# Performance work log

Measured on AMD Instinct MI355X. Metric: run time of the kernel, lower is better.

The kernel has to match this reference:

```python
import jax, jax.numpy as jnp
import numpy as np

B, C, H = 16, 256, 128   # batch, channels (in==out, depthwise), spatial
K, S, P = 3, 2, 1        # kernel, stride, padding (the shape-consistent _Transition config)
LEAVES = 4               # levels=2 -> levels**2


def dwconv(x, w, b, stride, pad):
    # depthwise conv: w is [C,1,K,K] (torch OIHW with groups=C)
    out = jax.lax.conv_general_dilated(
        x, w, (stride, stride), [(pad, pad), (pad, pad)],
        dimension_numbers=('NCHW', 'OIHW', 'NCHW'),
        feature_group_count=x.shape[1])
    return out + b[None, :, None, None]


def maxpool(x, k, s, p):
    # matches nn.MaxPool2d (padding acts as -inf for max)
    return jax.lax.reduce_window(
        x, -jnp.inf, jax.lax.max,
        (1, 1, k, k), (1, 1, s, s),
        [(0, 0), (0, 0), (p, p), (p, p)])


def setup_inputs() -> dict:
    key = jax.random.key(0)
    k0, k1, k2, k3 = jax.random.split(key, 4)
    std = (2.0 / (K * K * C)) ** 0.5  # matches the module's normal_(0, sqrt(2/n)) init
    x = jax.random.normal(k0, (B, C, H, H), jnp.float32)
    maxgate = jax.random.normal(k1, (C, 1, K, K), jnp.float32) * std
    pconvs = jax.random.normal(k2, (C, 1, K, K, LEAVES), jnp.float32) * std  # dw=True
    pgates = jax.random.normal(k3, (C, 1, K, K, 3), jnp.float32) * std       # b=False: (leaves+levels)//2 = 3
    mb = jnp.zeros((C,), jnp.float32)
    pbs = jnp.zeros((C, LEAVES), jnp.float32)
    gbs = jnp.zeros((C, 3), jnp.float32)
    return dict(x=x, maxgate=maxgate, mb=mb, pconvs=pconvs, pbs=pbs,
                pgates=pgates, gbs=gbs)


def reference(x, maxgate, mb, pconvs, pbs, pgates, gbs):
    # max branch: maxpool * depthwise gate conv
    out = maxpool(x, K, S, P) * dwconv(x, maxgate, mb, S, P)

    # leaf stage: 2 sigmoid-gated pool pairs (b=False -> gate2 = 1 - gate1)
    # NOTE: code indexes pgates.select(4, c*2) with gbs.select(1, c)
    leaves = []
    for c in range(LEAVES // 2):
        g1 = jax.nn.sigmoid(dwconv(x, pgates[..., 2 * c], gbs[:, c], S, P))
        p1 = dwconv(x, pconvs[..., 2 * c], pbs[:, 2 * c], S, P)
        p2 = dwconv(x, pconvs[..., 2 * c + 1], pbs[:, 2 * c + 1], S, P)
        leaves.append(g1 * p1)
        leaves.append((1.0 - g1) * p2)

    n0 = leaves[0] + leaves[1]
    n1 = leaves[2] + leaves[3]

    # node stage (kernel_size==3 -> no F.pad); b=False reuses pgates[..., leaves//2 + n] = pgates[...,2]
    g = jax.nn.sigmoid(dwconv(n0, pgates[..., LEAVES // 2], gbs[:, 2], 1, P))
    out = out + n0 * g + n1 * (1.0 - g)
    return out
```

## Files before the change

kernel.cpp:

```cpp
#include <hip/hip_runtime.h>
#include <math.h>

#define TB   256
#define HH   128
#define OHW  64
#define TR   16
#define XR   37
#define N0C  68
#define NBLK (16 * 256 * 4)
#define CPX  (NBLK / 8)

typedef float f32x2 __attribute__((ext_vector_type(2)));

__device__ __forceinline__ float sigmoidf(float z) {
    return 1.0f / (1.0f + __expf(-z));
}

__device__ __forceinline__ void gl2lds16(const float* g, float* l) {
    __builtin_amdgcn_global_load_lds(
        (const __attribute__((address_space(1))) void*)g,
        (__attribute__((address_space(3))) void*)l, 16, 0, 0);
}
__device__ __forceinline__ void gl2lds4(const float* g, float* l) {
    __builtin_amdgcn_global_load_lds(
        (const __attribute__((address_space(1))) void*)g,
        (__attribute__((address_space(3))) void*)l, 4, 0, 0);
}

__global__ __launch_bounds__(TB, 6) void fused_densenet_kernel(
    const float* __restrict__ x,
    const float* __restrict__ maxgate,
    const float* __restrict__ mb,
    const float* __restrict__ pconvs,
    const float* __restrict__ pbs,
    const float* __restrict__ pgates,
    const float* __restrict__ gbs,
    float* __restrict__ out)
{
    __shared__ float xs[XR][HH];
    __shared__ float n0s[TR + 2][N0C];

    const int t     = threadIdx.x;
    const int lane  = t & 63;
    const int wv    = t >> 6;
    const int bid   = blockIdx.x;
    const int l     = (bid & 7) * CPX + (bid >> 3);
    const int tile  = l & 3;
    const int plane = l >> 2;
    const int c     = plane & 255;
    const int r0    = tile * TR;

    float ws[7][9];
#pragma unroll
    for (int i = 0; i < 9; ++i) {
        ws[0][i] = maxgate[c * 9  + i];
        ws[1][i] = pconvs [c * 36 + i * 4 + 0];
        ws[2][i] = pconvs [c * 36 + i * 4 + 1];
        ws[3][i] = pconvs [c * 36 + i * 4 + 2];
        ws[4][i] = pconvs [c * 36 + i * 4 + 3];
        ws[5][i] = pgates [c * 27 + i * 3 + 0];
        ws[6][i] = pgates [c * 27 + i * 3 + 2];
    }
    const float bmax = mb[c];
    const float bp0 = pbs[c * 4 + 0], bp1 = pbs[c * 4 + 1];
    const float bp2 = pbs[c * 4 + 2], bp3 = pbs[c * 4 + 3];
    const float bg0 = gbs[c * 3 + 0];
    const float bg1 = gbs[c * 3 + 1];
    const float bg2 = gbs[c * 3 + 2];

    const float* xplane = x + (size_t)plane * (HH * HH);

    {
        const int ir0  = 2 * r0 - 3;
        const int lo   = ir0 < 0 ? 0 : ir0;
        const int hie  = ir0 + XR - 1;
        const int hi   = hie > HH - 1 ? HH - 1 : hie;
        const int ztop = lo - ir0;
        const int zbot = hie - hi;
        for (int i = t; i < ztop * HH; i += TB) (&xs[0][0])[i] = 0.f;
        for (int i = t; i < zbot * HH; i += TB) (&xs[XR - zbot][0])[i] = 0.f;
        const int    nfl  = (hi - lo + 1) * HH;
        const float* gsrc = xplane + lo * HH;
        float*       ldst = &xs[ztop][0];
        const int nchunk = nfl >> 8;
        for (int k = wv; k < nchunk; k += TB / 64)
            gl2lds16(gsrc + (k << 8) + lane * 4, ldst + (k << 8));
        if ((nfl & 255) && wv == 0) {
            const int off = nchunk << 8;
            gl2lds4(gsrc + off + lane,      ldst + off);
            gl2lds4(gsrc + off + 64 + lane, ldst + off + 64);
        }
        if (t < 2 * (TR + 2)) n0s[t >> 1][(t & 1) ? 66 : 1] = 0.f;
    }
    __syncthreads();

    if (t < 132) {
        const int hb  = (t >= 66);
        const int cc2 = hb ? t - 66 : t;
        const int gc  = cc2 - 1;
        const int gr  = hb ? r0 + TR : r0 - 1;
        float n0v = 0.f;
        if ((unsigned)gr < (unsigned)OHW && (unsigned)gc < (unsigned)OHW) {
            const int sb = hb ? 2 * TR + 2 : 0;
            float ag = 0.f, a0 = 0.f, a1 = 0.f;
#pragma unroll
            for (int dr = 0; dr < 3; ++dr) {
                const float* row = &xs[sb + dr][0];
                const float w0 = (gc > 0) ? row[2 * gc - 1] : 0.f;
                const float w1 = row[2 * gc];
                const float w2 = row[2 * gc + 1];
                ag += w0 * ws[5][3*dr] + w1 * ws[5][3*dr+1] + w2 * ws[5][3*dr+2];
                a0 += w0 * ws[1][3*dr] + w1 * ws[1][3*dr+1] + w2 * ws[1][3*dr+2];
                a1 += w0 * ws[2][3*dr] + w1 * ws[2][3*dr+1] + w2 * ws[2][3*dr+2];
            }
            const float sg = sigmoidf(ag + bg0);
            n0v = sg * (a0 + bp0) + (1.f - sg) * (a1 + bp1);
        }
        n0s[hb ? TR + 1 : 0][cc2 + 1] = n0v;
    }

    const int p  = t & 31;
    const int g0 = t >> 5;
    float out1[2][2], n1v[2][2];

#pragma unroll
    for (int k = 0; k < 2; ++k) {
        const int lr = g0 + 8 * k;
        const int gr = r0 + lr;
        float a[7][2];
#pragma unroll
        for (int ci = 0; ci < 7; ++ci) { a[ci][0] = 0.f; a[ci][1] = 0.f; }
        float mp0 = -INFINITY, mp1 = -INFINITY;
#pragma unroll
        for (int dr = 0; dr < 3; ++dr) {
            const float* row = &xs[2 * lr + 2 + dr][0];
            const float  v0 = (p > 0) ? row[4 * p - 1] : 0.f;
            const float4 vv = *reinterpret_cast<const float4*>(&row[4 * p]);
            const bool rowok = (gr > 0) | (dr > 0);
            const float h0 = fmaxf(fmaxf((p > 0) ? v0 : -INFINITY, vv.x), vv.y);
            const float h1 = fmaxf(fmaxf(vv.y, vv.z), vv.w);
            mp0 = fmaxf(mp0, rowok ? h0 : -INFINITY);
            mp1 = fmaxf(mp1, rowok ? h1 : -INFINITY);
#pragma unroll
            for (int ci = 0; ci < 7; ++ci) {
                a[ci][0] += v0   * ws[ci][3*dr] + vv.x * ws[ci][3*dr+1] + vv.y * ws[ci][3*dr+2];
                a[ci][1] += vv.y * ws[ci][3*dr] + vv.z * ws[ci][3*dr+1] + vv.w * ws[ci][3*dr+2];
            }
        }
        const float sg0a = sigmoidf(a[5][0] + bg0);
        const float sg0b = sigmoidf(a[5][1] + bg0);
        const float n0a = sg0a * (a[1][0] + bp0) + (1.f - sg0a) * (a[2][0] + bp1);
        const float n0b = sg0b * (a[1][1] + bp0) + (1.f - sg0b) * (a[2][1] + bp1);
        *reinterpret_cast<f32x2*>(&n0s[lr + 1][2 * p + 2]) = (f32x2){ n0a, n0b };
        const float sg1a = sigmoidf(a[6][0] + bg1);
        const float sg1b = sigmoidf(a[6][1] + bg1);
        n1v[k][0] = sg1a * (a[3][0] + bp2) + (1.f - sg1a) * (a[4][0] + bp3);
        n1v[k][1] = sg1b * (a[3][1] + bp2) + (1.f - sg1b) * (a[4][1] + bp3);
        out1[k][0] = mp0 * (a[0][0] + bmax);
        out1[k][1] = mp1 * (a[0][1] + bmax);
    }
    __syncthreads();

    float* oplane = out + (size_t)plane * (OHW * OHW);
#pragma unroll
    for (int k = 0; k < 2; ++k) {
        const int lr = g0 + 8 * k;
        float ag0 = 0.f, ag1 = 0.f, n0c0 = 0.f, n0c1 = 0.f;
#pragma unroll
        for (int dr = 0; dr < 3; ++dr) {
            const float e0  = n0s[lr + dr][2 * p + 1];
            const f32x2 mid = *reinterpret_cast<const f32x2*>(&n0s[lr + dr][2 * p + 2]);
            const float e3  = n0s[lr + dr][2 * p + 4];
            ag0 += e0    * ws[6][3*dr] + mid.x * ws[6][3*dr+1] + mid.y * ws[6][3*dr+2];
            ag1 += mid.x * ws[6][3*dr] + mid.y * ws[6][3*dr+1] + e3    * ws[6][3*dr+2];
            if (dr == 1) { n0c0 = mid.x; n0c1 = mid.y; }
        }
        const float ga = sigmoidf(ag0 + bg2);
        const float gb = sigmoidf(ag1 + bg2);
        f32x2 rv;
        rv.x = out1[k][0] + n0c0 * ga + n1v[k][0] * (1.f - ga);
        rv.y = out1[k][1] + n0c1 * gb + n1v[k][1] * (1.f - gb);
        __builtin_nontemporal_store(rv,
            reinterpret_cast<f32x2*>(oplane + (r0 + lr) * OHW + 2 * p));
    }
}

extern "C" void kernel_launch(void* const* d_in, const int* in_sizes, int n_in,
                              void* d_out, int out_size, void* d_ws, size_t ws_size,
                              hipStream_t stream) {
    const float* x       = (const float*)d_in[0];
    const float* maxgate = (const float*)d_in[1];
    const float* mb      = (const float*)d_in[2];
    const float* pconvs  = (const float*)d_in[3];
    const float* pbs     = (const float*)d_in[4];
    const float* pgates  = (const float*)d_in[5];
    const float* gbs     = (const float*)d_in[6];
    float* out           = (float*)d_out;

    fused_densenet_kernel<<<NBLK, TB, 0, stream>>>(
        x, maxgate, mb, pconvs, pbs, pgates, gbs, out);
}
```

Before: 81.29 us.

## Give each wavefront its own private x row slab to drop the load barrier

Each wave now loads its own overlapping slice of input rows into LDS (40 rows instead of 37, with duplicated halo rows). It waits only on its own vmcnt, which removes the first __syncthreads. The thread mapping also changes from 2 output columns per thread over 2 strided rows to 1 column per thread over 4 consecutive rows. Halo n0 rows are computed by waves 0 and 3 instead of a separate thread subset. This trades extra LDS traffic and redundant row loads for less block-wide synchronization and better wave independence.

After: 86.54 us. 6.5% more time.

```diff
diff --git a/kernel.cpp b/kernel.cpp
--- a/kernel.cpp
+++ b/kernel.cpp
@@ -5,7 +5,6 @@
 #define HH   128
 #define OHW  64
 #define TR   16
-#define XR   37
 #define N0C  68
 #define NBLK (16 * 256 * 4)
 #define CPX  (NBLK / 8)
@@ -37,11 +36,11 @@
     const float* __restrict__ gbs,
     float* __restrict__ out)
 {
-    __shared__ float xs[XR][HH];
+    __shared__ float xs[40][HH];
     __shared__ float n0s[TR + 2][N0C];
 
     const int t     = threadIdx.x;
-    const int lane  = t & 63;
+    const int cc    = t & 63;
     const int wv    = t >> 6;
     const int bid   = blockIdx.x;
     const int l     = (bid & 7) * CPX + (bid >> 3);
@@ -70,118 +69,119 @@
 
     const float* xplane = x + (size_t)plane * (HH * HH);
 
+    const int  wbase = (wv == 0) ? 0 : (11 + 9 * (wv - 1));
+    const int  ib0   = 2 * r0 + 8 * wv - ((wv == 0) ? 3 : 1);
+    const int  nw    = (wv == 0 || wv == 3) ? 11 : 9;
+    float*     base  = &xs[wbase][0];
     {
-        const int ir0  = 2 * r0 - 3;
-        const int lo   = ir0 < 0 ? 0 : ir0;
-        const int hie  = ir0 + XR - 1;
+        const int lo   = ib0 < 0 ? 0 : ib0;
+        const int hie  = ib0 + nw - 1;
         const int hi   = hie > HH - 1 ? HH - 1 : hie;
-        const int ztop = lo - ir0;
+        const int ztop = lo - ib0;
         const int zbot = hie - hi;
-        for (int i = t; i < ztop * HH; i += TB) (&xs[0][0])[i] = 0.f;
-        for (int i = t; i < zbot * HH; i += TB) (&xs[XR - zbot][0])[i] = 0.f;
+        for (int r = 0; r < ztop; ++r)
+            *reinterpret_cast<f32x2*>(&base[r * HH + 2 * cc]) = (f32x2){0.f, 0.f};
+        for (int r = 0; r < zbot; ++r)
+            *reinterpret_cast<f32x2*>(&base[(nw - 1 - r) * HH + 2 * cc]) = (f32x2){0.f, 0.f};
         const int    nfl  = (hi - lo + 1) * HH;
         const float* gsrc = xplane + lo * HH;
-        float*       ldst = &xs[ztop][0];
+        float*       ldst = base + ztop * HH;
         const int nchunk = nfl >> 8;
-        for (int k = wv; k < nchunk; k += TB / 64)
-            gl2lds16(gsrc + (k << 8) + lane * 4, ldst + (k << 8));
-        if ((nfl & 255) && wv == 0) {
+        for (int k = 0; k < nchunk; ++k)
+            gl2lds16(gsrc + (k << 8) + cc * 4, ldst + (k << 8));
+        if (nfl & 255) {
             const int off = nchunk << 8;
-            gl2lds4(gsrc + off + lane,      ldst + off);
-            gl2lds4(gsrc + off + 64 + lane, ldst + off + 64);
-        }
-        if (t < 2 * (TR + 2)) n0s[t >> 1][(t & 1) ? 66 : 1] = 0.f;
-    }
-    __syncthreads();
-
-    if (t < 132) {
-        const int hb  = (t >= 66);
-        const int cc2 = hb ? t - 66 : t;
-        const int gc  = cc2 - 1;
-        const int gr  = hb ? r0 + TR : r0 - 1;
+            gl2lds4(gsrc + off + cc,      ldst + off);
+            gl2lds4(gsrc + off + 64 + cc, ldst + off + 64);
+        }
+    }
+    if (wv == 1 && cc < 2 * (TR + 2)) n0s[cc >> 1][(cc & 1) ? 66 : 1] = 0.f;
+
+    asm volatile("s_waitcnt vmcnt(0)" ::: "memory");
+
+    const int roff = (wv == 0) ? 2 : 0;
+
+    if (wv == 0) {
         float n0v = 0.f;
-        if ((unsigned)gr < (unsigned)OHW && (unsigned)gc < (unsigned)OHW) {
-            const int sb = hb ? 2 * TR + 2 : 0;
-            float ag = 0.f, a0 = 0.f, a1 = 0.f;
+        if (r0 > 0) {
+            float ag = 0.f, q0 = 0.f, q1 = 0.f;
 #pragma unroll
             for (int dr = 0; dr < 3; ++dr) {
-                const float* row = &xs[sb + dr][0];
-                const float w0 = (gc > 0) ? row[2 * gc - 1] : 0.f;
-                const float w1 = row[2 * gc];
-                const float w2 = row[2 * gc + 1];
-                ag += w0 * ws[5][3*dr] + w1 * ws[5][3*dr+1] + w2 * ws[5][3*dr+2];
-                a0 += w0 * ws[1][3*dr] + w1 * ws[1][3*dr+1] + w2 * ws[1][3*dr+2];
-                a1 += w0 * ws[2][3*dr] + w1 * ws[2][3*dr+1] + w2 * ws[2][3*dr+2];
+                const float* row = &base[dr * HH];
+                const float v0 = cc ? row[2 * cc - 1] : 0.f;
+                const f32x2 d  = *reinterpret_cast<const f32x2*>(&row[2 * cc]);
+                ag += v0 * ws[5][3*dr] + d.x * ws[5][3*dr+1] + d.y * ws[5][3*dr+2];
+                q0 += v0 * ws[1][3*dr] + d.x * ws[1][3*dr+1] + d.y * ws[1][3*dr+2];
+                q1 += v0 * ws[2][3*dr] + d.x * ws[2][3*dr+1] + d.y * ws[2][3*dr+2];
             }
             const float sg = sigmoidf(ag + bg0);
-            n0v = sg * (a0 + bp0) + (1.f - sg) * (a1 + bp1);
-        }
-        n0s[hb ? TR + 1 : 0][cc2 + 1] = n0v;
-    }
-
-    const int p  = t & 31;
-    const int g0 = t >> 5;
-    float out1[2][2], n1v[2][2];
-
-#pragma unroll
-    for (int k = 0; k < 2; ++k) {
-        const int lr = g0 + 8 * k;
-        const int gr = r0 + lr;
-        float a[7][2];
-#pragma unroll
-        for (int ci = 0; ci < 7; ++ci) { a[ci][0] = 0.f; a[ci][1] = 0.f; }
-        float mp0 = -INFINITY, mp1 = -INFINITY;
+            n0v = sg * (q0 + bp0) + (1.f - sg) * (q1 + bp1);
+        }
+        n0s[0][cc + 2] = n0v;
+    }
+    if (wv == 3) {
+        float n0v = 0.f;
+        if (r0 + TR < OHW) {
+            float ag = 0.f, q0 = 0.f, q1 = 0.f;
+#pragma unroll
+            for (int dr = 0; dr < 3; ++dr) {
+                const float* row = &base[(8 + dr) * HH];
+                const float v0 = cc ? row[2 * cc - 1] : 0.f;
+                const f32x2 d  = *reinterpret_cast<const f32x2*>(&row[2 * cc]);
+                ag += v0 * ws[5][3*dr] + d.x * ws[5][3*dr+1] + d.y * ws[5][3*dr+2];
+                q0 += v0 * ws[1][3*dr] + d.x * ws[1][3*dr+1] + d.y * ws[1][3*dr+2];
+                q1 += v0 * ws[2][3*dr] + d.x * ws[2][3*dr+1] + d.y * ws[2][3*dr+2];
+            }
+            const float sg = sigmoidf(ag + bg0);
+            n0v = sg * (q0 + bp0) + (1.f - sg) * (q1 + bp1);
+        }
+        n0s[TR + 1][cc + 2] = n0v;
+    }
+
+    float o1[4], n1p[4];
+#pragma unroll
+    for (int k = 0; k < 4; ++k) {
+        const int lw = 2 * k + roff;
+        const int gr = r0 + 4 * wv + k;
+        float a[7];
+#pragma unroll
+        for (int ci = 0; ci < 7; ++ci) a[ci] = 0.f;
+        float mp = -INFINITY;
 #pragma unroll
         for (int dr = 0; dr < 3; ++dr) {
-            const float* row = &xs[2 * lr + 2 + dr][0];
-            const float  v0 = (p > 0) ? row[4 * p - 1] : 0.f;
-            const float4 vv = *reinterpret_cast<const float4*>(&row[4 * p]);
+            const float* row = &base[(lw + dr) * HH];
+            const float v0 = cc ? row[2 * cc - 1] : 0.f;
+            const f32x2 d  = *reinterpret_cast<const f32x2*>(&row[2 * cc]);
             const bool rowok = (gr > 0) | (dr > 0);
-            const float h0 = fmaxf(fmaxf((p > 0) ? v0 : -INFINITY, vv.x), vv.y);
-            const float h1 = fmaxf(fmaxf(vv.y, vv.z), vv.w);
-            mp0 = fmaxf(mp0, rowok ? h0 : -INFINITY);
-            mp1 = fmaxf(mp1, rowok ? h1 : -INFINITY);
-#pragma unroll
-            for (int ci = 0; ci < 7; ++ci) {
-                a[ci][0] += v0   * ws[ci][3*dr] + vv.x * ws[ci][3*dr+1] + vv.y * ws[ci][3*dr+2];
-                a[ci][1] += vv.y * ws[ci][3*dr] + vv.z * ws[ci][3*dr+1] + vv.w * ws[ci][3*dr+2];
-            }
-        }
-        const float sg0a = sigmoidf(a[5][0] + bg0);
-        const float sg0b = sigmoidf(a[5][1] + bg0);
-        const float n0a = sg0a * (a[1][0] + bp0) + (1.f - sg0a) * (a[2][0] + bp1);
-        const float n0b = sg0b * (a[1][1] + bp0) + (1.f - sg0b) * (a[2][1] + bp1);
-        *reinterpret_cast<f32x2*>(&n0s[lr + 1][2 * p + 2]) = (f32x2){ n0a, n0b };
-        const float sg1a = sigmoidf(a[6][0] + bg1);
-        const float sg1b = sigmoidf(a[6][1] + bg1);
-        n1v[k][0] = sg1a * (a[3][0] + bp2) + (1.f - sg1a) * (a[4][0] + bp3);
-        n1v[k][1] = sg1b * (a[3][1] + bp2) + (1.f - sg1b) * (a[4][1] + bp3);
-        out1[k][0] = mp0 * (a[0][0] + bmax);
-        out1[k][1] = mp1 * (a[0][1] + bmax);
+            const float h = fmaxf(fmaxf(cc ? v0 : -INFINITY, d.x), d.y);
+            mp = fmaxf(mp, rowok ? h : -INFINITY);
+#pragma unroll
+            for (int ci = 0; ci < 7; ++ci)
+                a[ci] += v0 * ws[ci][3*dr] + d.x * ws[ci][3*dr+1] + d.y * ws[ci][3*dr+2];
+        }
+        const float sg0 = sigmoidf(a[5] + bg0);
+        n0s[4 * wv + k + 1][cc + 2] = sg0 * (a[1] + bp0) + (1.f - sg0) * (a[2] + bp1);
+        const float sg1 = sigmoidf(a[6] + bg1);
+        n1p[k] = sg1 * (a[3] + bp2) + (1.f - sg1) * (a[4] + bp3);
+        o1[k]  = mp * (a[0] + bmax);
     }
     __syncthreads();
 
     float* oplane = out + (size_t)plane * (OHW * OHW);
 #pragma unroll
-    for (int k = 0; k < 2; ++k) {
-        const int lr = g0 + 8 * k;
-        float ag0 = 0.f, ag1 = 0.f, n0c0 = 0.f, n0c1 = 0.f;
+    for (int k = 0; k < 4; ++k) {
+        const int lr = 4 * wv + k;
+        float ag = 0.f;
 #pragma unroll
         for (int dr = 0; dr < 3; ++dr) {
-            const float e0  = n0s[lr + dr][2 * p + 1];
-            const f32x2 mid = *reinterpret_cast<const f32x2*>(&n0s[lr + dr][2 * p + 2]);
-            const float e3  = n0s[lr + dr][2 * p + 4];
-            ag0 += e0    * ws[6][3*dr] + mid.x * ws[6][3*dr+1] + mid.y * ws[6][3*dr+2];
-            ag1 += mid.x * ws[6][3*dr] + mid.y * ws[6][3*dr+1] + e3    * ws[6][3*dr+2];
-            if (dr == 1) { n0c0 = mid.x; n0c1 = mid.y; }
-        }
-        const float ga = sigmoidf(ag0 + bg2);
-        const float gb = sigmoidf(ag1 + bg2);
-        f32x2 rv;
-        rv.x = out1[k][0] + n0c0 * ga + n1v[k][0] * (1.f - ga);
-        rv.y = out1[k][1] + n0c1 * gb + n1v[k][1] * (1.f - gb);
-        __builtin_nontemporal_store(rv,
-            reinterpret_cast<f32x2*>(oplane + (r0 + lr) * OHW + 2 * p));
+            const float* nr = &n0s[lr + dr][0];
+            ag += nr[cc + 1] * ws[6][3*dr] + nr[cc + 2] * ws[6][3*dr+1]
+                + nr[cc + 3] * ws[6][3*dr+2];
+        }
+        const float g   = sigmoidf(ag + bg2);
+        const float n0c = n0s[lr + 1][cc + 2];
+        __builtin_nontemporal_store(o1[k] + n0c * g + n1p[k] * (1.f - g),
+                                    oplane + (r0 + lr) * OHW + cc);
     }
 }
 
```

## Read input directly from global memory instead of staging x tile in LDS

Applied to the files above, without the earlier changes.

Removes the 37x128 LDS staging buffer and its async global-to-LDS copy plus barrier, so each thread loads its input rows straight from global memory (relying on L1/L2 for the overlapping rows). The row mapping changes so each 32-thread group handles two adjacent output rows, which share one input row. Launch bounds go from 6 to 8 blocks per CU, now that LDS use is much smaller. The trade-off is more global load instructions and redundant reads of overlapping rows in exchange for higher occupancy and no staging synchronization.

After: 237.0 us. 2.92x slower.

```diff
diff --git a/kernel.cpp b/kernel.cpp
--- a/kernel.cpp
+++ b/kernel.cpp
@@ -5,7 +5,6 @@
 #define HH   128
 #define OHW  64
 #define TR   16
-#define XR   37
 #define N0C  68
 #define NBLK (16 * 256 * 4)
 #define CPX  (NBLK / 8)
@@ -16,18 +15,7 @@
     return 1.0f / (1.0f + __expf(-z));
 }
 
-__device__ __forceinline__ void gl2lds16(const float* g, float* l) {
-    __builtin_amdgcn_global_load_lds(
-        (const __attribute__((address_space(1))) void*)g,
-        (__attribute__((address_space(3))) void*)l, 16, 0, 0);
-}
-__device__ __forceinline__ void gl2lds4(const float* g, float* l) {
-    __builtin_amdgcn_global_load_lds(
-        (const __attribute__((address_space(1))) void*)g,
-        (__attribute__((address_space(3))) void*)l, 4, 0, 0);
-}
-
-__global__ __launch_bounds__(TB, 6) void fused_densenet_kernel(
+__global__ __launch_bounds__(TB, 8) void fused_densenet_kernel(
     const float* __restrict__ x,
     const float* __restrict__ maxgate,
     const float* __restrict__ mb,
@@ -37,18 +25,17 @@
     const float* __restrict__ gbs,
     float* __restrict__ out)
 {
-    __shared__ float xs[XR][HH];
     __shared__ float n0s[TR + 2][N0C];
 
     const int t     = threadIdx.x;
-    const int lane  = t & 63;
-    const int wv    = t >> 6;
     const int bid   = blockIdx.x;
     const int l     = (bid & 7) * CPX + (bid >> 3);
     const int tile  = l & 3;
     const int plane = l >> 2;
     const int c     = plane & 255;
     const int r0    = tile * TR;
+    const int p     = t & 31;
+    const int q     = t >> 5;
 
     float ws[7][9];
 #pragma unroll
@@ -70,29 +57,7 @@
 
     const float* xplane = x + (size_t)plane * (HH * HH);
 
-    {
-        const int ir0  = 2 * r0 - 3;
-        const int lo   = ir0 < 0 ? 0 : ir0;
-        const int hie  = ir0 + XR - 1;
-        const int hi   = hie > HH - 1 ? HH - 1 : hie;
-        const int ztop = lo - ir0;
-        const int zbot = hie - hi;
-        for (int i = t; i < ztop * HH; i += TB) (&xs[0][0])[i] = 0.f;
-        for (int i = t; i < zbot * HH; i += TB) (&xs[XR - zbot][0])[i] = 0.f;
-        const int    nfl  = (hi - lo + 1) * HH;
-        const float* gsrc = xplane + lo * HH;
-        float*       ldst = &xs[ztop][0];
-        const int nchunk = nfl >> 8;
-        for (int k = wv; k < nchunk; k += TB / 64)
-            gl2lds16(gsrc + (k << 8) + lane * 4, ldst + (k << 8));
-        if ((nfl & 255) && wv == 0) {
-            const int off = nchunk << 8;
-            gl2lds4(gsrc + off + lane,      ldst + off);
-            gl2lds4(gsrc + off + 64 + lane, ldst + off + 64);
-        }
-        if (t < 2 * (TR + 2)) n0s[t >> 1][(t & 1) ? 66 : 1] = 0.f;
-    }
-    __syncthreads();
+    if (t < 2 * (TR + 2)) n0s[t >> 1][(t & 1) ? 66 : 1] = 0.f;
 
     if (t < 132) {
         const int hb  = (t >= 66);
@@ -101,17 +66,18 @@
         const int gr  = hb ? r0 + TR : r0 - 1;
         float n0v = 0.f;
         if ((unsigned)gr < (unsigned)OHW && (unsigned)gc < (unsigned)OHW) {
-            const int sb = hb ? 2 * TR + 2 : 0;
             float ag = 0.f, a0 = 0.f, a1 = 0.f;
 #pragma unroll
             for (int dr = 0; dr < 3; ++dr) {
-                const float* row = &xs[sb + dr][0];
-                const float w0 = (gc > 0) ? row[2 * gc - 1] : 0.f;
-                const float w1 = row[2 * gc];
-                const float w2 = row[2 * gc + 1];
-                ag += w0 * ws[5][3*dr] + w1 * ws[5][3*dr+1] + w2 * ws[5][3*dr+2];
-                a0 += w0 * ws[1][3*dr] + w1 * ws[1][3*dr+1] + w2 * ws[1][3*dr+2];
-                a1 += w0 * ws[2][3*dr] + w1 * ws[2][3*dr+1] + w2 * ws[2][3*dr+2];
+                const int ir = 2 * gr - 1 + dr;
+                if (ir >= 0) {
+                    const float* row = xplane + ir * HH;
+                    const float w0 = (gc > 0) ? row[2 * gc - 1] : 0.f;
+                    const f32x2 d  = *reinterpret_cast<const f32x2*>(&row[2 * gc]);
+                    ag += w0 * ws[5][3*dr] + d.x * ws[5][3*dr+1] + d.y * ws[5][3*dr+2];
+                    a0 += w0 * ws[1][3*dr] + d.x * ws[1][3*dr+1] + d.y * ws[1][3*dr+2];
+                    a1 += w0 * ws[2][3*dr] + d.x * ws[2][3*dr+1] + d.y * ws[2][3*dr+2];
+                }
             }
             const float sg = sigmoidf(ag + bg0);
             n0v = sg * (a0 + bp0) + (1.f - sg) * (a1 + bp1);
@@ -119,13 +85,10 @@
         n0s[hb ? TR + 1 : 0][cc2 + 1] = n0v;
     }
 
-    const int p  = t & 31;
-    const int g0 = t >> 5;
     float out1[2][2], n1v[2][2];
-
 #pragma unroll
     for (int k = 0; k < 2; ++k) {
-        const int lr = g0 + 8 * k;
+        const int lr = 2 * q + k;
         const int gr = r0 + lr;
         float a[7][2];
 #pragma unroll
@@ -133,14 +96,19 @@
         float mp0 = -INFINITY, mp1 = -INFINITY;
 #pragma unroll
         for (int dr = 0; dr < 3; ++dr) {
-            const float* row = &xs[2 * lr + 2 + dr][0];
-            const float  v0 = (p > 0) ? row[4 * p - 1] : 0.f;
-            const float4 vv = *reinterpret_cast<const float4*>(&row[4 * p]);
-            const bool rowok = (gr > 0) | (dr > 0);
+            const int ir = 2 * gr - 1 + dr;
+            const bool rok = (ir >= 0);
+            const float* row = xplane + ir * HH;
+            float  v0 = 0.f;
+            float4 vv = make_float4(0.f, 0.f, 0.f, 0.f);
+            if (rok) {
+                if (p > 0) v0 = row[4 * p - 1];
+                vv = *reinterpret_cast<const float4*>(&row[4 * p]);
+            }
             const float h0 = fmaxf(fmaxf((p > 0) ? v0 : -INFINITY, vv.x), vv.y);
             const float h1 = fmaxf(fmaxf(vv.y, vv.z), vv.w);
-            mp0 = fmaxf(mp0, rowok ? h0 : -INFINITY);
-            mp1 = fmaxf(mp1, rowok ? h1 : -INFINITY);
+            mp0 = fmaxf(mp0, rok ? h0 : -INFINITY);
+            mp1 = fmaxf(mp1, rok ? h1 : -INFINITY);
 #pragma unroll
             for (int ci = 0; ci < 7; ++ci) {
                 a[ci][0] += v0   * ws[ci][3*dr] + vv.x * ws[ci][3*dr+1] + vv.y * ws[ci][3*dr+2];
@@ -164,7 +132,7 @@
     float* oplane = out + (size_t)plane * (OHW * OHW);
 #pragma unroll
     for (int k = 0; k < 2; ++k) {
-        const int lr = g0 + 8 * k;
+        const int lr = 2 * q + k;
         float ag0 = 0.f, ag1 = 0.f, n0c0 = 0.f, n0c1 = 0.f;
 #pragma unroll
         for (int dr = 0; dr < 3; ++dr) {
```
